# Performance work log

Hardware: AMD Instinct MI355X
Metric: run time of the kernel (lower is better)

The kernel has to match this reference:

```python
import jax, jax.numpy as jnp
import numpy as np
import math

MARGIN = 0.5
SCALE = 64.0
CURVATURE = 1.0
COS_M = math.cos(MARGIN)
SIN_M = math.sin(MARGIN)
TH = math.cos(math.pi - MARGIN)
MM = math.sin(math.pi - MARGIN) * MARGIN

B, D, C = 2048, 512, 16384


def setup_inputs() -> dict:
    key = jax.random.key(0)
    k1, k2, k3 = jax.random.split(key, 3)
    embeddings = jax.random.normal(k1, (B, D), dtype=jnp.float32) * 0.05  # roughly inside the ball
    labels = jax.random.randint(k2, (B,), 0, C)
    # xavier_uniform for [C, D]
    limit = math.sqrt(6.0 / (C + D))
    weight = jax.random.uniform(k3, (C, D), dtype=jnp.float32, minval=-limit, maxval=limit)
    return {"embeddings": embeddings, "labels": labels, "weight": weight}


def _exp_map_zero(v, c):
    sqrt_c = c ** 0.5
    v_norm = jnp.maximum(jnp.linalg.norm(v, axis=-1, keepdims=True), 1e-7)
    return jnp.tanh(sqrt_c * v_norm) * v / (sqrt_c * v_norm)


def reference(embeddings, labels, weight):
    c = CURVATURE
    # class prototypes mapped onto the Poincare ball, clipped to radius 0.95
    proto = _exp_map_zero(weight, c)                                  # [C, D]
    proto_norm = jnp.linalg.norm(proto, axis=-1, keepdims=True)
    proto = jnp.where(proto_norm > 0.95, proto * 0.95 / proto_norm, proto)

    x = embeddings                                                     # [B, D]
    x_sq = jnp.sum(x * x, axis=-1)                                    # [B]
    y_sq = jnp.sum(proto * proto, axis=-1)                            # [C]
    xy = x @ proto.T                                                  # [B, C]
    diff_sq = jnp.maximum(x_sq[:, None] + y_sq[None, :] - 2.0 * xy, 0.0)

    x_sq_c = jnp.minimum(x_sq, 1.0 - 1e-5)
    y_sq_c = jnp.minimum(y_sq, 1.0 - 1e-5)
    denom = (1.0 - c * x_sq_c)[:, None] * (1.0 - c * y_sq_c)[None, :]
    arg = 1.0 + 2.0 * c * diff_sq / jnp.maximum(denom, 1e-7)
    dists = jnp.arccosh(jnp.maximum(arg, 1.0 + 1e-7)) / (c ** 0.5)    # [B, C]

    sims = jnp.exp(-dists)
    cosine = jnp.clip(2.0 * sims - 1.0, -1.0, 1.0)
    sine = jnp.sqrt(jnp.maximum(1.0 - cosine * cosine, 1e-7))
    phi = cosine * COS_M - sine * SIN_M
    phi = jnp.where(cosine > TH, phi, cosine - MM)

    one_hot = jax.nn.one_hot(labels, cosine.shape[1], dtype=cosine.dtype)
    logits = (one_hot * phi + (1.0 - one_hot) * cosine) * SCALE        # [B, C]

    logp = jax.nn.log_softmax(logits, axis=-1)
    loss = -jnp.mean(jnp.take_along_axis(logp, labels[:, None], axis=1))
    return loss
```

## Files before the change

kernel.cpp:

```cpp
#include <hip/hip_runtime.h>
#include <hip/hip_bf16.h>
#include <math.h>

#define Bn 2048
#define Dn 512
#define Cn 16384

typedef __bf16 v8bf __attribute__((ext_vector_type(8)));
typedef float v4f __attribute__((ext_vector_type(4)));

#define WAIT_VM4()      asm volatile("s_waitcnt vmcnt(4)" ::: "memory")
#define WAIT_VM0()      asm volatile("s_waitcnt vmcnt(0)" ::: "memory")
#define RAW_BAR()       asm volatile("s_barrier" ::: "memory")
#define LGKM0_BAR()     asm volatile("s_waitcnt lgkmcnt(0)\n\ts_barrier" ::: "memory")

__device__ __forceinline__ void async16(const void* g, void* l) {
  __builtin_amdgcn_global_load_lds(
      (const __attribute__((address_space(1))) char*)g,
      (__attribute__((address_space(3))) char*)l, 16, 0, 0);
}

__global__ __launch_bounds__(256) void prep_kernel(
    const float* __restrict__ w, const float* __restrict__ x,
    __hip_bfloat16* __restrict__ wbf, __hip_bfloat16* __restrict__ xbf,
    float* __restrict__ fscale, float* __restrict__ ysqA, float* __restrict__ yrA,
    float* __restrict__ xsA, float* __restrict__ xrA)
{
  int gw = (blockIdx.x * 256 + threadIdx.x) >> 6;
  int lane = threadIdx.x & 63;
  bool isW = gw < Cn;
  const float* src = isW ? (w + (size_t)gw * Dn) : (x + (size_t)(gw - Cn) * Dn);
  const float4* s4 = (const float4*)src;
  float4 a = s4[lane * 2], b = s4[lane * 2 + 1];
  float ss = a.x * a.x + a.y * a.y + a.z * a.z + a.w * a.w
           + b.x * b.x + b.y * b.y + b.z * b.z + b.w * b.w;
  #pragma unroll
  for (int d = 1; d < 64; d <<= 1) ss += __shfl_xor(ss, d);

  union { __hip_bfloat16 h[8]; int4 i4; } u;
  u.h[0] = __float2bfloat16(a.x); u.h[1] = __float2bfloat16(a.y);
  u.h[2] = __float2bfloat16(a.z); u.h[3] = __float2bfloat16(a.w);
  u.h[4] = __float2bfloat16(b.x); u.h[5] = __float2bfloat16(b.y);
  u.h[6] = __float2bfloat16(b.z); u.h[7] = __float2bfloat16(b.w);
  __hip_bfloat16* dst = isW ? (wbf + (size_t)gw * Dn) : (xbf + (size_t)(gw - Cn) * Dn);
  ((int4*)dst)[lane] = u.i4;

  if (lane == 0) {
    if (isW) {
      float n = fmaxf(sqrtf(ss), 1e-7f);
      float t = tanhf(n);
      float tc = fminf(t, 0.95f);
      fscale[gw] = tc / n;
      float ys = tc * tc;
      ysqA[gw] = ys;
      yrA[gw] = 1.f / (1.f - fminf(ys, 1.f - 1e-5f));
    } else {
      int r = gw - Cn;
      xsA[r] = ss;
      xrA[r] = 1.f / (1.f - fminf(ss, 1.f - 1e-5f));
    }
  }
}

__global__ __launch_bounds__(256) void gemm_kernel(
    const __hip_bfloat16* __restrict__ xbf, const __hip_bfloat16* __restrict__ wbf,
    const float* __restrict__ fscale, const float* __restrict__ ysqA,
    const float* __restrict__ yrA, const float* __restrict__ xsA,
    const float* __restrict__ xrA, float* __restrict__ partials)
{
  __shared__ int4 ldsv[2048];
  char* lds = (char*)ldsv;

  const int bid = blockIdx.x;
  const int xcd = bid & 7;
  const int loc = bid >> 3;
  const int mt  = loc & 15;
  const int nt  = (xcd << 4) | (loc >> 4);
  const int mBase = mt * 128;
  const int nBase = nt * 128;
  const int tid = threadIdx.x;
  const int lane = tid & 63;
  const int wave = tid >> 6;
  const int quad = lane >> 4;
  const int l16 = lane & 15;
  const int waveM = wave >> 1;
  const int waveN = wave & 1;

  v4f acc[4][4];
  #pragma unroll
  for (int i = 0; i < 4; ++i)
    #pragma unroll
    for (int j = 0; j < 4; ++j)
      acc[i][j] = (v4f){0.f, 0.f, 0.f, 0.f};

  const int s0 = tid, s1 = tid + 256;
  const int r0 = s0 >> 2, c0 = (s0 & 3) ^ (r0 & 3);
  const int r1 = s1 >> 2, c1 = (s1 & 3) ^ (r1 & 3);
  const char* gA0 = (const char*)xbf + (size_t)(mBase + r0) * (Dn * 2) + c0 * 16;
  const char* gA1 = (const char*)xbf + (size_t)(mBase + r1) * (Dn * 2) + c1 * 16;
  const char* gW0 = (const char*)wbf + (size_t)(nBase + r0) * (Dn * 2) + c0 * 16;
  const char* gW1 = (const char*)wbf + (size_t)(nBase + r1) * (Dn * 2) + c1 * 16;
  const int lo0 = s0 * 16, lo1 = s1 * 16;

  int aoffs[4], boffs[4];
  #pragma unroll
  for (int i = 0; i < 4; ++i) {
    int ra = waveM * 64 + i * 16 + l16;
    aoffs[i] = ra * 64 + ((quad ^ (ra & 3)) * 16);
    int rb = waveN * 64 + i * 16 + l16;
    boffs[i] = rb * 64 + ((quad ^ (rb & 3)) * 16);
  }

  #pragma unroll
  for (int t = 0; t < 2; ++t) {
    char* b = lds + t * 16384;
    async16(gA0 + t * 64, b + lo0);
    async16(gA1 + t * 64, b + lo1);
    async16(gW0 + t * 64, b + 8192 + lo0);
    async16(gW1 + t * 64, b + 8192 + lo1);
  }

  #pragma unroll
  for (int kt = 0; kt < 16; ++kt) {
    const int cur = kt & 1;
    if (kt < 15) { WAIT_VM4(); } else { WAIT_VM0(); }
    RAW_BAR();
    char* Ab = lds + cur * 16384;
    char* Wb = Ab + 8192;
    v8bf af[4], bfr[4];
    #pragma unroll
    for (int i = 0; i < 4; ++i) af[i] = *(const v8bf*)(Ab + aoffs[i]);
    #pragma unroll
    for (int j = 0; j < 4; ++j) bfr[j] = *(const v8bf*)(Wb + boffs[j]);
    LGKM0_BAR();
    if (kt + 2 < 16) {
      async16(gA0 + (kt + 2) * 64, Ab + lo0);
      async16(gA1 + (kt + 2) * 64, Ab + lo1);
      async16(gW0 + (kt + 2) * 64, Wb + lo0);
      async16(gW1 + (kt + 2) * 64, Wb + lo1);
    }
    #pragma unroll
    for (int i = 0; i < 4; ++i)
      #pragma unroll
      for (int j = 0; j < 4; ++j)
        acc[i][j] = __builtin_amdgcn_mfma_f32_16x16x32_bf16(af[i], bfr[j], acc[i][j], 0, 0, 0);
  }

  float ysqj[4], yrj[4], gj[4];
  #pragma unroll
  for (int j = 0; j < 4; ++j) {
    int col = nBase + waveN * 64 + j * 16 + l16;
    gj[j] = -2.f * fscale[col];
    ysqj[j] = ysqA[col];
    yrj[j] = yrA[col];
  }
  #pragma unroll
  for (int i = 0; i < 4; ++i) {
    #pragma unroll
    for (int r = 0; r < 4; ++r) {
      int row = mBase + waveM * 64 + i * 16 + quad * 4 + r;
      float xs = xsA[row];
      float xr2 = 2.f * xrA[row];
      float partial = 0.f;
      if (xs >= 0.99999f) {
        #pragma unroll
        for (int j = 0; j < 4; ++j) {
          float d = fmaxf(fmaf(gj[j], acc[i][j][r], xs + ysqj[j]), 0.f);
          float z = fmaf(d, xr2 * yrj[j], 1.f);
          float u = 64.f * __builtin_amdgcn_rcpf(z);
          partial += fmaf(u, fmaf(0.5f, u, 1.f), 1.f);
        }
      } else {
        #pragma unroll
        for (int j = 0; j < 4; ++j) {
          float d = fmaxf(fmaf(gj[j], acc[i][j][r], xs + ysqj[j]), 0.f);
          float z = fmaf(d, xr2 * yrj[j], 1.f);
          float sq = sqrtf(fmaf(z, z, -1.f));
          float u = 128.f * __builtin_amdgcn_rcpf(z + sq);
          partial += __expf(u);
        }
      }
      partial += __shfl_xor(partial, 1);
      partial += __shfl_xor(partial, 2);
      partial += __shfl_xor(partial, 4);
      partial += __shfl_xor(partial, 8);
      if (l16 == 0) partials[(size_t)row * 256 + nt * 2 + waveN] = partial;
    }
  }
}

__global__ __launch_bounds__(256) void final_kernel(
    const float* __restrict__ x, const float* __restrict__ w,
    const int* __restrict__ labels, const float* __restrict__ fscale,
    const float* __restrict__ ysqA, const float* __restrict__ yrA,
    const float* __restrict__ xsA, const float* __restrict__ xrA,
    const float* __restrict__ partials, float* __restrict__ out)
{
  int row = blockIdx.x * 4 + (threadIdx.x >> 6);
  int lane = threadIdx.x & 63;
  const float* pr = partials + (size_t)row * 256;
  float sum = pr[lane] + pr[lane + 64] + pr[lane + 128] + pr[lane + 192];

  int lab = labels[row];
  const float4* xv = (const float4*)(x + (size_t)row * Dn);
  const float4* wv = (const float4*)(w + (size_t)lab * Dn);
  float4 a0 = xv[lane * 2], a1 = xv[lane * 2 + 1];
  float4 b0 = wv[lane * 2], b1 = wv[lane * 2 + 1];
  float dot = a0.x * b0.x + a0.y * b0.y + a0.z * b0.z + a0.w * b0.w
            + a1.x * b1.x + a1.y * b1.y + a1.z * b1.z + a1.w * b1.w;
  #pragma unroll
  for (int d = 1; d < 64; d <<= 1) {
    sum += __shfl_xor(sum, d);
    dot += __shfl_xor(dot, d);
  }

  __shared__ float red[4];
  if (lane == 0) {
    float xy = fscale[lab] * dot;
    float diff = fmaxf(xsA[row] + ysqA[lab] - 2.f * xy, 0.f);
    float z = fmaf(2.f * diff, xrA[row] * yrA[lab], 1.f);
    float sq = sqrtf(fmaf(z, z, -1.f));
    float sims = 1.f / (z + sq);
    float u_lab = 128.f * sims;
    float cosv = fmaf(2.f, sims, -1.f);
    float sine = sqrtf(fmaxf(fmaf(-cosv, cosv, 1.f), 1e-7f));
    float phi = (cosv > -0.8775825619f)
                    ? (cosv * 0.8775825619f - sine * 0.4794255386f)
                    : (cosv - 0.2397127693f);
    float e_lab = __expf(u_lab);
    float e_phi = __expf(fminf(64.f * phi + 64.f, 80.f));
    red[threadIdx.x >> 6] = logf(sum - e_lab + e_phi) - 64.f * phi - 64.f;
  }
  __syncthreads();
  if (threadIdx.x == 0)
    atomicAdd(out, (red[0] + red[1] + red[2] + red[3]) * (1.f / (float)Bn));
}

extern "C" void kernel_launch(void* const* d_in, const int* in_sizes, int n_in,
                              void* d_out, int out_size, void* d_ws, size_t ws_size,
                              hipStream_t stream) {
  (void)in_sizes; (void)n_in; (void)out_size; (void)ws_size;
  const float* emb = (const float*)d_in[0];
  const int* labels = (const int*)d_in[1];
  const float* weight = (const float*)d_in[2];
  float* out = (float*)d_out;

  char* p = (char*)d_ws;
  __hip_bfloat16* wbf = (__hip_bfloat16*)p; p += (size_t)Cn * Dn * 2;
  __hip_bfloat16* xbf = (__hip_bfloat16*)p; p += (size_t)Bn * Dn * 2;
  float* fscale = (float*)p; p += (size_t)Cn * 4;
  float* ysqA  = (float*)p; p += (size_t)Cn * 4;
  float* yrA   = (float*)p; p += (size_t)Cn * 4;
  float* xsA   = (float*)p; p += (size_t)Bn * 4;
  float* xrA   = (float*)p; p += (size_t)Bn * 4;
  float* partials = (float*)p; p += (size_t)Bn * 256 * 4;

  hipMemsetAsync(out, 0, sizeof(float), stream);
  prep_kernel<<<(Cn + Bn) / 4, 256, 0, stream>>>(weight, emb, wbf, xbf, fscale, ysqA, yrA, xsA, xrA);
  gemm_kernel<<<(Bn / 128) * (Cn / 128), 256, 0, stream>>>(
      xbf, wbf, fscale, ysqA, yrA, xsA, xrA, partials);
  final_kernel<<<Bn / 4, 256, 0, stream>>>(emb, weight, labels, fscale, ysqA, yrA, xsA, xrA, partials, out);
}
```

Before: 141.6 us.

## Widen GEMM tile to 128x256 and change LDS swizzle

```diff
diff --git a/kernel.cpp b/kernel.cpp
--- a/kernel.cpp
+++ b/kernel.cpp
@@ -9,10 +9,10 @@
 typedef __bf16 v8bf __attribute__((ext_vector_type(8)));
 typedef float v4f __attribute__((ext_vector_type(4)));
 
-#define WAIT_VM4()      asm volatile("s_waitcnt vmcnt(4)" ::: "memory")
-#define WAIT_VM0()      asm volatile("s_waitcnt vmcnt(0)" ::: "memory")
-#define RAW_BAR()       asm volatile("s_barrier" ::: "memory")
-#define LGKM0_BAR()     asm volatile("s_waitcnt lgkmcnt(0)\n\ts_barrier" ::: "memory")
+#define WAIT_VM6()  asm volatile("s_waitcnt vmcnt(6)" ::: "memory")
+#define WAIT_VM0()  asm volatile("s_waitcnt vmcnt(0)" ::: "memory")
+#define RAW_BAR()   asm volatile("s_barrier" ::: "memory")
+#define LGKM0_BAR() asm volatile("s_waitcnt lgkmcnt(0)\n\ts_barrier" ::: "memory")
 
 __device__ __forceinline__ void async16(const void* g, void* l) {
   __builtin_amdgcn_global_load_lds(
@@ -62,22 +62,22 @@
   }
 }
 
-__global__ __launch_bounds__(256) void gemm_kernel(
+__global__ __launch_bounds__(256, 2) void gemm_kernel(
     const __hip_bfloat16* __restrict__ xbf, const __hip_bfloat16* __restrict__ wbf,
     const float* __restrict__ fscale, const float* __restrict__ ysqA,
     const float* __restrict__ yrA, const float* __restrict__ xsA,
     const float* __restrict__ xrA, float* __restrict__ partials)
 {
-  __shared__ int4 ldsv[2048];
+  __shared__ int4 ldsv[3072];
   char* lds = (char*)ldsv;
 
   const int bid = blockIdx.x;
   const int xcd = bid & 7;
   const int loc = bid >> 3;
   const int mt  = loc & 15;
-  const int nt  = (xcd << 4) | (loc >> 4);
+  const int nt  = (xcd << 3) | (loc >> 4);
   const int mBase = mt * 128;
-  const int nBase = nt * 128;
+  const int nBase = nt * 256;
   const int tid = threadIdx.x;
   const int lane = tid & 63;
   const int wave = tid >> 6;
@@ -86,70 +86,80 @@
   const int waveM = wave >> 1;
   const int waveN = wave & 1;
 
-  v4f acc[4][4];
+  v4f acc[4][8];
   #pragma unroll
   for (int i = 0; i < 4; ++i)
     #pragma unroll
-    for (int j = 0; j < 4; ++j)
+    for (int j = 0; j < 8; ++j)
       acc[i][j] = (v4f){0.f, 0.f, 0.f, 0.f};
 
-  const int s0 = tid, s1 = tid + 256;
-  const int r0 = s0 >> 2, c0 = (s0 & 3) ^ (r0 & 3);
-  const int r1 = s1 >> 2, c1 = (s1 & 3) ^ (r1 & 3);
-  const char* gA0 = (const char*)xbf + (size_t)(mBase + r0) * (Dn * 2) + c0 * 16;
-  const char* gA1 = (const char*)xbf + (size_t)(mBase + r1) * (Dn * 2) + c1 * 16;
-  const char* gW0 = (const char*)wbf + (size_t)(nBase + r0) * (Dn * 2) + c0 * 16;
-  const char* gW1 = (const char*)wbf + (size_t)(nBase + r1) * (Dn * 2) + c1 * 16;
-  const int lo0 = s0 * 16, lo1 = s1 * 16;
-
-  int aoffs[4], boffs[4];
+  const int sA0 = tid, sA1 = tid + 256;
+  const int rA0 = sA0 >> 2, cA0 = (sA0 & 3) ^ ((rA0 >> 1) & 3);
+  const int rA1 = sA1 >> 2, cA1 = (sA1 & 3) ^ ((rA1 >> 1) & 3);
+  const char* gA0 = (const char*)xbf + (size_t)(mBase + rA0) * (Dn * 2) + cA0 * 16;
+  const char* gA1 = (const char*)xbf + (size_t)(mBase + rA1) * (Dn * 2) + cA1 * 16;
+  const int loA0 = sA0 * 16, loA1 = sA1 * 16;
+  const char* gW[4]; int loW[4];
+  #pragma unroll
+  for (int p = 0; p < 4; ++p) {
+    int s = tid + p * 256;
+    int r = s >> 2, c = (s & 3) ^ ((r >> 1) & 3);
+    gW[p] = (const char*)wbf + (size_t)(nBase + r) * (Dn * 2) + c * 16;
+    loW[p] = s * 16;
+  }
+
+  int aoffs[4], boffs[8];
   #pragma unroll
   for (int i = 0; i < 4; ++i) {
     int ra = waveM * 64 + i * 16 + l16;
-    aoffs[i] = ra * 64 + ((quad ^ (ra & 3)) * 16);
-    int rb = waveN * 64 + i * 16 + l16;
-    boffs[i] = rb * 64 + ((quad ^ (rb & 3)) * 16);
+    aoffs[i] = ra * 64 + ((quad ^ ((ra >> 1) & 3)) * 16);
+  }
+  #pragma unroll
+  for (int j = 0; j < 8; ++j) {
+    int rb = waveN * 128 + j * 16 + l16;
+    boffs[j] = rb * 64 + ((quad ^ ((rb >> 1) & 3)) * 16);
   }
 
   #pragma unroll
   for (int t = 0; t < 2; ++t) {
-    char* b = lds + t * 16384;
-    async16(gA0 + t * 64, b + lo0);
-    async16(gA1 + t * 64, b + lo1);
-    async16(gW0 + t * 64, b + 8192 + lo0);
-    async16(gW1 + t * 64, b + 8192 + lo1);
+    char* Ab = lds + t * 24576;
+    char* Wb = Ab + 8192;
+    async16(gA0 + t * 64, Ab + loA0);
+    async16(gA1 + t * 64, Ab + loA1);
+    #pragma unroll
+    for (int p = 0; p < 4; ++p) async16(gW[p] + t * 64, Wb + loW[p]);
   }
 
   #pragma unroll
   for (int kt = 0; kt < 16; ++kt) {
     const int cur = kt & 1;
-    if (kt < 15) { WAIT_VM4(); } else { WAIT_VM0(); }
+    if (kt < 15) { WAIT_VM6(); } else { WAIT_VM0(); }
     RAW_BAR();
-    char* Ab = lds + cur * 16384;
+    char* Ab = lds + cur * 24576;
     char* Wb = Ab + 8192;
-    v8bf af[4], bfr[4];
+    v8bf af[4], bfv[8];
     #pragma unroll
     for (int i = 0; i < 4; ++i) af[i] = *(const v8bf*)(Ab + aoffs[i]);
     #pragma unroll
-    for (int j = 0; j < 4; ++j) bfr[j] = *(const v8bf*)(Wb + boffs[j]);
+    for (int j = 0; j < 8; ++j) bfv[j] = *(const v8bf*)(Wb + boffs[j]);
     LGKM0_BAR();
     if (kt + 2 < 16) {
-      async16(gA0 + (kt + 2) * 64, Ab + lo0);
-      async16(gA1 + (kt + 2) * 64, Ab + lo1);
-      async16(gW0 + (kt + 2) * 64, Wb + lo0);
-      async16(gW1 + (kt + 2) * 64, Wb + lo1);
+      async16(gA0 + (kt + 2) * 64, Ab + loA0);
+      async16(gA1 + (kt + 2) * 64, Ab + loA1);
+      #pragma unroll
+      for (int p = 0; p < 4; ++p) async16(gW[p] + (kt + 2) * 64, Wb + loW[p]);
     }
     #pragma unroll
     for (int i = 0; i < 4; ++i)
       #pragma unroll
-      for (int j = 0; j < 4; ++j)
-        acc[i][j] = __builtin_amdgcn_mfma_f32_16x16x32_bf16(af[i], bfr[j], acc[i][j], 0, 0, 0);
-  }
-
-  float ysqj[4], yrj[4], gj[4];
-  #pragma unroll
-  for (int j = 0; j < 4; ++j) {
-    int col = nBase + waveN * 64 + j * 16 + l16;
+      for (int j = 0; j < 8; ++j)
+        acc[i][j] = __builtin_amdgcn_mfma_f32_16x16x32_bf16(af[i], bfv[j], acc[i][j], 0, 0, 0);
+  }
+
+  float ysqj[8], yrj[8], gj[8];
+  #pragma unroll
+  for (int j = 0; j < 8; ++j) {
+    int col = nBase + waveN * 128 + j * 16 + l16;
     gj[j] = -2.f * fscale[col];
     ysqj[j] = ysqA[col];
     yrj[j] = yrA[col];
@@ -164,7 +174,7 @@
       float partial = 0.f;
       if (xs >= 0.99999f) {
         #pragma unroll
-        for (int j = 0; j < 4; ++j) {
+        for (int j = 0; j < 8; ++j) {
           float d = fmaxf(fmaf(gj[j], acc[i][j][r], xs + ysqj[j]), 0.f);
           float z = fmaf(d, xr2 * yrj[j], 1.f);
           float u = 64.f * __builtin_amdgcn_rcpf(z);
@@ -172,7 +182,7 @@
         }
       } else {
         #pragma unroll
-        for (int j = 0; j < 4; ++j) {
+        for (int j = 0; j < 8; ++j) {
           float d = fmaxf(fmaf(gj[j], acc[i][j][r], xs + ysqj[j]), 0.f);
           float z = fmaf(d, xr2 * yrj[j], 1.f);
           float sq = sqrtf(fmaf(z, z, -1.f));
@@ -184,7 +194,7 @@
       partial += __shfl_xor(partial, 2);
       partial += __shfl_xor(partial, 4);
       partial += __shfl_xor(partial, 8);
-      if (l16 == 0) partials[(size_t)row * 256 + nt * 2 + waveN] = partial;
+      if (l16 == 0) partials[(size_t)row * 128 + nt * 2 + waveN] = partial;
     }
   }
 }
@@ -198,8 +208,8 @@
 {
   int row = blockIdx.x * 4 + (threadIdx.x >> 6);
   int lane = threadIdx.x & 63;
-  const float* pr = partials + (size_t)row * 256;
-  float sum = pr[lane] + pr[lane + 64] + pr[lane + 128] + pr[lane + 192];
+  const float* pr = partials + (size_t)row * 128;
+  float sum = pr[lane] + pr[lane + 64];
 
   int lab = labels[row];
   const float4* xv = (const float4*)(x + (size_t)row * Dn);
@@ -253,11 +263,11 @@
   float* yrA   = (float*)p; p += (size_t)Cn * 4;
   float* xsA   = (float*)p; p += (size_t)Bn * 4;
   float* xrA   = (float*)p; p += (size_t)Bn * 4;
-  float* partials = (float*)p; p += (size_t)Bn * 256 * 4;
+  float* partials = (float*)p; p += (size_t)Bn * 128 * 4;
 
   hipMemsetAsync(out, 0, sizeof(float), stream);
   prep_kernel<<<(Cn + Bn) / 4, 256, 0, stream>>>(weight, emb, wbf, xbf, fscale, ysqA, yrA, xsA, xrA);
-  gemm_kernel<<<(Bn / 128) * (Cn / 128), 256, 0, stream>>>(
+  gemm_kernel<<<(Bn / 128) * (Cn / 256), 256, 0, stream>>>(
       xbf, wbf, fscale, ysqA, yrA, xsA, xrA, partials);
   final_kernel<<<Bn / 4, 256, 0, stream>>>(emb, weight, labels, fscale, ysqA, yrA, xsA, xrA, partials, out);
 }
```

New measurement: 137.5 us. -2.9%, faster.

## Switch GEMM operands to scaled FP8 with triple-buffered LDS pipeline

Applied to the files above, without the earlier changes.

```diff
diff --git a/kernel.cpp b/kernel.cpp
--- a/kernel.cpp
+++ b/kernel.cpp
@@ -6,13 +6,11 @@
 #define Dn 512
 #define Cn 16384
 
-typedef __bf16 v8bf __attribute__((ext_vector_type(8)));
 typedef float v4f __attribute__((ext_vector_type(4)));
 
-#define WAIT_VM4()      asm volatile("s_waitcnt vmcnt(4)" ::: "memory")
-#define WAIT_VM0()      asm volatile("s_waitcnt vmcnt(0)" ::: "memory")
-#define RAW_BAR()       asm volatile("s_barrier" ::: "memory")
-#define LGKM0_BAR()     asm volatile("s_waitcnt lgkmcnt(0)\n\ts_barrier" ::: "memory")
+#define WAIT_VM4()  asm volatile("s_waitcnt vmcnt(4)" ::: "memory")
+#define WAIT_VM0()  asm volatile("s_waitcnt vmcnt(0)" ::: "memory")
+#define LGKM0_BAR() asm volatile("s_waitcnt lgkmcnt(0)\n\ts_barrier" ::: "memory")
 
 __device__ __forceinline__ void async16(const void* g, void* l) {
   __builtin_amdgcn_global_load_lds(
@@ -22,7 +20,7 @@
 
 __global__ __launch_bounds__(256) void prep_kernel(
     const float* __restrict__ w, const float* __restrict__ x,
-    __hip_bfloat16* __restrict__ wbf, __hip_bfloat16* __restrict__ xbf,
+    char* __restrict__ wq8, char* __restrict__ xq8,
     float* __restrict__ fscale, float* __restrict__ ysqA, float* __restrict__ yrA,
     float* __restrict__ xsA, float* __restrict__ xrA)
 {
@@ -37,13 +35,12 @@
   #pragma unroll
   for (int d = 1; d < 64; d <<= 1) ss += __shfl_xor(ss, d);
 
-  union { __hip_bfloat16 h[8]; int4 i4; } u;
-  u.h[0] = __float2bfloat16(a.x); u.h[1] = __float2bfloat16(a.y);
-  u.h[2] = __float2bfloat16(a.z); u.h[3] = __float2bfloat16(a.w);
-  u.h[4] = __float2bfloat16(b.x); u.h[5] = __float2bfloat16(b.y);
-  u.h[6] = __float2bfloat16(b.z); u.h[7] = __float2bfloat16(b.w);
-  __hip_bfloat16* dst = isW ? (wbf + (size_t)gw * Dn) : (xbf + (size_t)(gw - Cn) * Dn);
-  ((int4*)dst)[lane] = u.i4;
+  int w0 = __builtin_amdgcn_cvt_pk_fp8_f32(a.x * 16.f, a.y * 16.f, 0, false);
+  w0     = __builtin_amdgcn_cvt_pk_fp8_f32(a.z * 16.f, a.w * 16.f, w0, true);
+  int w1 = __builtin_amdgcn_cvt_pk_fp8_f32(b.x * 16.f, b.y * 16.f, 0, false);
+  w1     = __builtin_amdgcn_cvt_pk_fp8_f32(b.z * 16.f, b.w * 16.f, w1, true);
+  char* dst = isW ? (wq8 + (size_t)gw * Dn) : (xq8 + (size_t)(gw - Cn) * Dn);
+  ((int2*)dst)[lane] = make_int2(w0, w1);
 
   if (lane == 0) {
     if (isW) {
@@ -62,13 +59,13 @@
   }
 }
 
-__global__ __launch_bounds__(256) void gemm_kernel(
-    const __hip_bfloat16* __restrict__ xbf, const __hip_bfloat16* __restrict__ wbf,
+__global__ __launch_bounds__(256, 3) void gemm_kernel(
+    const char* __restrict__ xq8, const char* __restrict__ wq8,
     const float* __restrict__ fscale, const float* __restrict__ ysqA,
     const float* __restrict__ yrA, const float* __restrict__ xsA,
     const float* __restrict__ xrA, float* __restrict__ partials)
 {
-  __shared__ int4 ldsv[2048];
+  __shared__ int4 ldsv[3072];
   char* lds = (char*)ldsv;
 
   const int bid = blockIdx.x;
@@ -94,63 +91,71 @@
       acc[i][j] = (v4f){0.f, 0.f, 0.f, 0.f};
 
   const int s0 = tid, s1 = tid + 256;
-  const int r0 = s0 >> 2, c0 = (s0 & 3) ^ (r0 & 3);
-  const int r1 = s1 >> 2, c1 = (s1 & 3) ^ (r1 & 3);
-  const char* gA0 = (const char*)xbf + (size_t)(mBase + r0) * (Dn * 2) + c0 * 16;
-  const char* gA1 = (const char*)xbf + (size_t)(mBase + r1) * (Dn * 2) + c1 * 16;
-  const char* gW0 = (const char*)wbf + (size_t)(nBase + r0) * (Dn * 2) + c0 * 16;
-  const char* gW1 = (const char*)wbf + (size_t)(nBase + r1) * (Dn * 2) + c1 * 16;
+  const int r0 = s0 >> 2, c0 = (s0 & 3) ^ ((r0 >> 1) & 3);
+  const int r1 = s1 >> 2, c1 = (s1 & 3) ^ ((r1 >> 1) & 3);
+  const char* gA0 = xq8 + (size_t)(mBase + r0) * Dn + c0 * 16;
+  const char* gA1 = xq8 + (size_t)(mBase + r1) * Dn + c1 * 16;
+  const char* gW0 = wq8 + (size_t)(nBase + r0) * Dn + c0 * 16;
+  const char* gW1 = wq8 + (size_t)(nBase + r1) * Dn + c1 * 16;
   const int lo0 = s0 * 16, lo1 = s1 * 16;
 
-  int aoffs[4], boffs[4];
-  #pragma unroll
-  for (int i = 0; i < 4; ++i) {
-    int ra = waveM * 64 + i * 16 + l16;
-    aoffs[i] = ra * 64 + ((quad ^ (ra & 3)) * 16);
-    int rb = waveN * 64 + i * 16 + l16;
-    boffs[i] = rb * 64 + ((quad ^ (rb & 3)) * 16);
+  const int kx = (l16 >> 1) & 3;
+  int aoff[2], boff[2];
+  #pragma unroll
+  for (int s = 0; s < 2; ++s) {
+    int chunk = (2 * s + (quad >> 1)) ^ kx;
+    aoff[s] = (waveM * 64 + l16) * 64 + chunk * 16 + (quad & 1) * 8;
+    boff[s] = (waveN * 64 + l16) * 64 + chunk * 16 + (quad & 1) * 8;
   }
 
   #pragma unroll
   for (int t = 0; t < 2; ++t) {
-    char* b = lds + t * 16384;
-    async16(gA0 + t * 64, b + lo0);
-    async16(gA1 + t * 64, b + lo1);
-    async16(gW0 + t * 64, b + 8192 + lo0);
-    async16(gW1 + t * 64, b + 8192 + lo1);
-  }
-
-  #pragma unroll
-  for (int kt = 0; kt < 16; ++kt) {
-    const int cur = kt & 1;
-    if (kt < 15) { WAIT_VM4(); } else { WAIT_VM0(); }
-    RAW_BAR();
+    char* Ab = lds + t * 16384;
+    char* Wb = Ab + 8192;
+    async16(gA0 + t * 64, Ab + lo0);
+    async16(gA1 + t * 64, Ab + lo1);
+    async16(gW0 + t * 64, Wb + lo0);
+    async16(gW1 + t * 64, Wb + lo1);
+  }
+
+  #pragma unroll
+  for (int kt = 0; kt < 8; ++kt) {
+    const int cur = kt % 3;
+    if (kt < 7) { WAIT_VM4(); } else { WAIT_VM0(); }
+    LGKM0_BAR();
     char* Ab = lds + cur * 16384;
     char* Wb = Ab + 8192;
-    v8bf af[4], bfr[4];
-    #pragma unroll
-    for (int i = 0; i < 4; ++i) af[i] = *(const v8bf*)(Ab + aoffs[i]);
-    #pragma unroll
-    for (int j = 0; j < 4; ++j) bfr[j] = *(const v8bf*)(Wb + boffs[j]);
-    LGKM0_BAR();
-    if (kt + 2 < 16) {
-      async16(gA0 + (kt + 2) * 64, Ab + lo0);
-      async16(gA1 + (kt + 2) * 64, Ab + lo1);
-      async16(gW0 + (kt + 2) * 64, Wb + lo0);
-      async16(gW1 + (kt + 2) * 64, Wb + lo1);
-    }
-    #pragma unroll
-    for (int i = 0; i < 4; ++i)
+    if (kt + 2 < 8) {
+      const int nx = (kt + 2) % 3;
+      char* An = lds + nx * 16384;
+      char* Wn = An + 8192;
+      async16(gA0 + (kt + 2) * 64, An + lo0);
+      async16(gA1 + (kt + 2) * 64, An + lo1);
+      async16(gW0 + (kt + 2) * 64, Wn + lo0);
+      async16(gW1 + (kt + 2) * 64, Wn + lo1);
+    }
+    long af[4][2], bf[4][2];
+    #pragma unroll
+    for (int s = 0; s < 2; ++s) {
       #pragma unroll
-      for (int j = 0; j < 4; ++j)
-        acc[i][j] = __builtin_amdgcn_mfma_f32_16x16x32_bf16(af[i], bfr[j], acc[i][j], 0, 0, 0);
+      for (int i = 0; i < 4; ++i) af[i][s] = *(const long*)(Ab + aoff[s] + i * 1024);
+      #pragma unroll
+      for (int j = 0; j < 4; ++j) bf[j][s] = *(const long*)(Wb + boff[s] + j * 1024);
+    }
+    #pragma unroll
+    for (int s = 0; s < 2; ++s)
+      #pragma unroll
+      for (int i = 0; i < 4; ++i)
+        #pragma unroll
+        for (int j = 0; j < 4; ++j)
+          acc[i][j] = __builtin_amdgcn_mfma_f32_16x16x32_fp8_fp8(af[i][s], bf[j][s], acc[i][j], 0, 0, 0);
   }
 
   float ysqj[4], yrj[4], gj[4];
   #pragma unroll
   for (int j = 0; j < 4; ++j) {
     int col = nBase + waveN * 64 + j * 16 + l16;
-    gj[j] = -2.f * fscale[col];
+    gj[j] = -2.f * fscale[col] * (1.f / 256.f);
     ysqj[j] = ysqA[col];
     yrj[j] = yrA[col];
   }
@@ -246,8 +251,8 @@
   float* out = (float*)d_out;
 
   char* p = (char*)d_ws;
-  __hip_bfloat16* wbf = (__hip_bfloat16*)p; p += (size_t)Cn * Dn * 2;
-  __hip_bfloat16* xbf = (__hip_bfloat16*)p; p += (size_t)Bn * Dn * 2;
+  char* wq8 = p; p += (size_t)Cn * Dn;
+  char* xq8 = p; p += (size_t)Bn * Dn;
   float* fscale = (float*)p; p += (size_t)Cn * 4;
   float* ysqA  = (float*)p; p += (size_t)Cn * 4;
   float* yrA   = (float*)p; p += (size_t)Cn * 4;
@@ -256,8 +261,8 @@
   float* partials = (float*)p; p += (size_t)Bn * 256 * 4;
 
   hipMemsetAsync(out, 0, sizeof(float), stream);
-  prep_kernel<<<(Cn + Bn) / 4, 256, 0, stream>>>(weight, emb, wbf, xbf, fscale, ysqA, yrA, xsA, xrA);
+  prep_kernel<<<(Cn + Bn) / 4, 256, 0, stream>>>(weight, emb, wq8, xq8, fscale, ysqA, yrA, xsA, xrA);
   gemm_kernel<<<(Bn / 128) * (Cn / 128), 256, 0, stream>>>(
-      xbf, wbf, fscale, ysqA, yrA, xsA, xrA, partials);
+      xq8, wq8, fscale, ysqA, yrA, xsA, xrA, partials);
   final_kernel<<<Bn / 4, 256, 0, stream>>>(emb, weight, labels, fscale, ysqA, yrA, xsA, xrA, partials, out);
 }
```

Result: faster. 130.0 us (-8.2%).
